# Performance work log

Hardware: AMD Instinct MI355X
Metric: run time of the kernel (lower is better)

## Reference

```python
import jax, jax.numpy as jnp
import numpy as np

B = 4
POINT_NUM = 50000
N_VOXELS = 150000
FEAT_DIM = 256


def setup_inputs() -> dict:
    key = jax.random.key(0)
    k1, k2, k3, k4 = jax.random.split(key, 4)
    backbone_features = jax.random.normal(k1, (N_VOXELS, FEAT_DIM), dtype=jnp.float32)
    quantize2original = jax.random.randint(k2, (B * POINT_NUM,), 0, N_VOXELS, dtype=jnp.int64)
    # Conv1d(FEAT_DIM, 2, kernel_size=1) weight [2, FEAT_DIM] and bias [2]
    fan_in = FEAT_DIM
    bound = 1.0 / np.sqrt(fan_in)
    w_scoring = jax.random.uniform(k3, (2, FEAT_DIM), minval=-bound, maxval=bound, dtype=jnp.float32)
    b_scoring = jax.random.uniform(k4, (2,), minval=-bound, maxval=bound, dtype=jnp.float32)
    return {
        'backbone_features': backbone_features,
        'quantize2original': quantize2original,
        'w_scoring': w_scoring,
        'b_scoring': b_scoring,
    }


def reference(backbone_features, quantize2original, w_scoring, b_scoring):
    # Gather realign: voxel features -> original point order  [B*P, C]
    seed_features = backbone_features[quantize2original]
    # [B, P, C] -> [B, C, P]
    seed_features = seed_features.reshape(B, POINT_NUM, FEAT_DIM).transpose(0, 2, 1)
    # 1x1 Conv1d scoring head: [B, 2, P]
    suction_score = jnp.einsum('oc,bcp->bop', w_scoring, seed_features) + b_scoring[None, :, None]
    seal_score_pred = suction_score[:, 0]    # [B, P]
    wrench_score_pred = suction_score[:, 1]  # [B, P]
    return seal_score_pred, wrench_score_pred
```

## Files before the change

kernel.cpp:

```cpp
#include <hip/hip_runtime.h>

#define BATCH 4
#define POINT_NUM 50000
#define NPTS (BATCH * POINT_NUM)
#define NVOX 150000
#define FEAT 256

__global__ __launch_bounds__(256) void project_kernel(
    const float* __restrict__ feat,
    const float* __restrict__ w,
    const float* __restrict__ bias,
    float* __restrict__ s0,
    float* __restrict__ s1)
{
    const int wave = (blockIdx.x * blockDim.x + threadIdx.x) >> 6;
    const int lane = threadIdx.x & 63;
    if (wave >= NVOX) return;

    const float4 w0 = ((const float4*)(w))[lane];
    const float4 w1 = ((const float4*)(w + FEAT))[lane];
    const float4 f  = ((const float4*)(feat + (size_t)wave * FEAT))[lane];

    float a = f.x * w0.x + f.y * w0.y + f.z * w0.z + f.w * w0.w;
    float b = f.x * w1.x + f.y * w1.y + f.z * w1.z + f.w * w1.w;

    #pragma unroll
    for (int off = 32; off > 0; off >>= 1) {
        a += __shfl_down(a, off, 64);
        b += __shfl_down(b, off, 64);
    }

    if (lane == 0) {
        s0[wave] = a + bias[0];
        s1[wave] = b + bias[1];
    }
}

__global__ __launch_bounds__(256) void gather_kernel(
    const int* __restrict__ idx,
    const float* __restrict__ s0,
    const float* __restrict__ s1,
    float* __restrict__ out)
{
    const int p = blockIdx.x * blockDim.x + threadIdx.x;
    if (p >= NPTS) return;
    const int v = idx[p];
    out[p]        = s0[v];
    out[NPTS + p] = s1[v];
}

extern "C" void kernel_launch(void* const* d_in, const int* in_sizes, int n_in,
                              void* d_out, int out_size, void* d_ws, size_t ws_size,
                              hipStream_t stream) {
    const float* feat = (const float*)d_in[0];
    const int*   idx  = (const int*)d_in[1];
    const float* w    = (const float*)d_in[2];
    const float* bias = (const float*)d_in[3];
    float* out = (float*)d_out;

    float* s0 = (float*)d_ws;
    float* s1 = s0 + NVOX;

    const int blocks1 = (NVOX * 64 + 255) / 256;
    project_kernel<<<blocks1, 256, 0, stream>>>(feat, w, bias, s0, s1);

    const int blocks2 = (NPTS + 255) / 256;
    gather_kernel<<<blocks2, 256, 0, stream>>>(idx, s0, s1, out);
}
```

Measured before the change: 215.5 us.

## Fuse projection and gather into one per-point gather-dot kernel

Replaces the two-pass scheme (project every voxel, then gather scores per point) with one kernel where each wave gathers its point's voxel feature row and computes both dot products directly. This removes the intermediate score buffer and the second launch. In exchange it reads feature rows per point rather than per voxel, which raises total feature traffic and makes it random-access, and it adds a dependent index load before the feature load.

```diff
diff --git a/kernel.cpp b/kernel.cpp
--- a/kernel.cpp
+++ b/kernel.cpp
@@ -6,20 +6,23 @@
 #define NVOX 150000
 #define FEAT 256
 
-__global__ __launch_bounds__(256) void project_kernel(
+__global__ __launch_bounds__(256) void fused_score_kernel(
     const float* __restrict__ feat,
+    const int*   __restrict__ idx,
     const float* __restrict__ w,
     const float* __restrict__ bias,
-    float* __restrict__ s0,
-    float* __restrict__ s1)
+    float* __restrict__ out)
 {
     const int wave = (blockIdx.x * blockDim.x + threadIdx.x) >> 6;
     const int lane = threadIdx.x & 63;
-    if (wave >= NVOX) return;
+    if (wave >= NPTS) return;
+
+    const int v = idx[wave];
 
     const float4 w0 = ((const float4*)(w))[lane];
     const float4 w1 = ((const float4*)(w + FEAT))[lane];
-    const float4 f  = ((const float4*)(feat + (size_t)wave * FEAT))[lane];
+
+    const float4 f = ((const float4*)(feat + (size_t)v * FEAT))[lane];
 
     float a = f.x * w0.x + f.y * w0.y + f.z * w0.z + f.w * w0.w;
     float b = f.x * w1.x + f.y * w1.y + f.z * w1.z + f.w * w1.w;
@@ -31,22 +34,9 @@
     }
 
     if (lane == 0) {
-        s0[wave] = a + bias[0];
-        s1[wave] = b + bias[1];
+        out[wave]        = a + bias[0];
+        out[NPTS + wave] = b + bias[1];
     }
-}
-
-__global__ __launch_bounds__(256) void gather_kernel(
-    const int* __restrict__ idx,
-    const float* __restrict__ s0,
-    const float* __restrict__ s1,
-    float* __restrict__ out)
-{
-    const int p = blockIdx.x * blockDim.x + threadIdx.x;
-    if (p >= NPTS) return;
-    const int v = idx[p];
-    out[p]        = s0[v];
-    out[NPTS + p] = s1[v];
 }
 
 extern "C" void kernel_launch(void* const* d_in, const int* in_sizes, int n_in,
@@ -58,12 +48,8 @@
     const float* bias = (const float*)d_in[3];
     float* out = (float*)d_out;
 
-    float* s0 = (float*)d_ws;
-    float* s1 = s0 + NVOX;
+    (void)d_ws; (void)ws_size;
 
-    const int blocks1 = (NVOX * 64 + 255) / 256;
-    project_kernel<<<blocks1, 256, 0, stream>>>(feat, w, bias, s0, s1);
-
-    const int blocks2 = (NPTS + 255) / 256;
-    gather_kernel<<<blocks2, 256, 0, stream>>>(idx, s0, s1, out);
+    const int blocks = (NPTS * 64 + 255) / 256;
+    fused_score_kernel<<<blocks, 256, 0, stream>>>(feat, idx, w, bias, out);
 }
```

Result: slower. 238.3 us (+10.6%).
